# Kernel optimization log

Hardware: AMD Instinct MI355X
Metric: run time of the kernel (lower is better)

## Reference

```python
import jax, jax.numpy as jnp
import numpy as np

MOMENTUM = 0.9


def setup_inputs() -> dict:
    key = jax.random.key(0)
    k1, k2, k3, k4 = jax.random.split(key, 4)
    B, D, C = 524288, 256, 1000
    x = jax.random.normal(k1, (B, D), dtype=jnp.float32)
    l = jax.random.randint(k2, (B,), 0, C, dtype=jnp.int64)
    center_img = jax.random.normal(k3, (C, D), dtype=jnp.float32)
    center_skt = jax.random.normal(k4, (C, D), dtype=jnp.float32)
    return {"x": x, "l": l, "center_img": center_img, "center_skt": center_skt}


def reference(x, l, center_img, center_skt):
    # Faithful vectorized version of CenterAlignment.forward (modality='img').
    # The per-sample Python scatter-add loop -> segment_sum over fixed num_classes;
    # torch.unique's data-dependent class set -> boolean 'present' mask.
    C = center_img.shape[0]
    counts = jax.ops.segment_sum(jnp.ones(x.shape[0], dtype=x.dtype), l, num_segments=C)  # [C]
    sums = jax.ops.segment_sum(x, l, num_segments=C)                                      # [C, D]
    present = counts > 0
    mean = sums / jnp.maximum(counts, 1.0)[:, None]  # per-class mean (safe div for absent classes)
    # momentum update + L2 renormalization, only for classes present in the batch
    upd = center_img * MOMENTUM + mean * (1.0 - MOMENTUM)
    upd = upd / jnp.linalg.norm(upd, axis=1, keepdims=True)
    new_img = jnp.where(present[:, None], upd, center_img)
    # align_loss with alpha=2: mean over present classes of ||c_img - c_skt||^2
    diff = new_img - center_skt
    sq = jnp.sum(diff * diff, axis=1)  # [C]
    n_present = jnp.maximum(jnp.sum(present.astype(x.dtype)), 1.0)
    loss = jnp.sum(jnp.where(present, sq, 0.0)) / n_present
    return loss
```

## Files before the change

kernel.cpp:

```cpp
#include <hip/hip_runtime.h>

#define MAXC    1000
#define DSUB    32
#define LSTR    33
#define THREADS 1024
#define NCHUNK  32
#define FIXS    1048576.0f
#define INVFIXS (1.0f / 1048576.0f)

template <int MODE>
__global__ __launch_bounds__(THREADS) void scatter_kernel(
    const float* __restrict__ x, const int* __restrict__ l,
    float* __restrict__ part, float* __restrict__ cnt_part,
    int* __restrict__ sums_i, int* __restrict__ cnt_i,
    int B, int D, int C, int chunk)
{
    __shared__ int lsum[MAXC * LSTR];
    __shared__ int lcnt[MAXC];

    for (int i = threadIdx.x; i < MAXC * LSTR; i += THREADS) lsum[i] = 0;
    for (int i = threadIdx.x; i < MAXC; i += THREADS) lcnt[i] = 0;
    __syncthreads();

    const bool doCount = (blockIdx.y == 0);
    const int dbase = blockIdx.y * DSUB;
    const int q     = threadIdx.x & 7;
    const int srel  = threadIdx.x >> 3;
    const int STEP  = THREADS >> 3;
    const int DV    = D >> 2;
    const int qb    = (dbase >> 2) + q;

    const float4* __restrict__ x4 = (const float4*)x;

    const int s0 = blockIdx.x * chunk;
    const int s1 = min(B, s0 + chunk);

    int s = s0 + srel;
    for (; s + 3 * STEP < s1; s += 4 * STEP) {
        int c0 = l[s];
        int c1 = l[s + STEP];
        int c2 = l[s + 2 * STEP];
        int c3 = l[s + 3 * STEP];
        float4 v0 = x4[(size_t)s * DV + qb];
        float4 v1 = x4[(size_t)(s + STEP) * DV + qb];
        float4 v2 = x4[(size_t)(s + 2 * STEP) * DV + qb];
        float4 v3 = x4[(size_t)(s + 3 * STEP) * DV + qb];
        const int b0 = c0 * LSTR + (q << 2);
        const int b1 = c1 * LSTR + (q << 2);
        const int b2 = c2 * LSTR + (q << 2);
        const int b3 = c3 * LSTR + (q << 2);
        atomicAdd(&lsum[b0 + 0], __float2int_rn(v0.x * FIXS));
        atomicAdd(&lsum[b0 + 1], __float2int_rn(v0.y * FIXS));
        atomicAdd(&lsum[b0 + 2], __float2int_rn(v0.z * FIXS));
        atomicAdd(&lsum[b0 + 3], __float2int_rn(v0.w * FIXS));
        atomicAdd(&lsum[b1 + 0], __float2int_rn(v1.x * FIXS));
        atomicAdd(&lsum[b1 + 1], __float2int_rn(v1.y * FIXS));
        atomicAdd(&lsum[b1 + 2], __float2int_rn(v1.z * FIXS));
        atomicAdd(&lsum[b1 + 3], __float2int_rn(v1.w * FIXS));
        atomicAdd(&lsum[b2 + 0], __float2int_rn(v2.x * FIXS));
        atomicAdd(&lsum[b2 + 1], __float2int_rn(v2.y * FIXS));
        atomicAdd(&lsum[b2 + 2], __float2int_rn(v2.z * FIXS));
        atomicAdd(&lsum[b2 + 3], __float2int_rn(v2.w * FIXS));
        atomicAdd(&lsum[b3 + 0], __float2int_rn(v3.x * FIXS));
        atomicAdd(&lsum[b3 + 1], __float2int_rn(v3.y * FIXS));
        atomicAdd(&lsum[b3 + 2], __float2int_rn(v3.z * FIXS));
        atomicAdd(&lsum[b3 + 3], __float2int_rn(v3.w * FIXS));
        if (doCount && q == 0) {
            atomicAdd(&lcnt[c0], 1);
            atomicAdd(&lcnt[c1], 1);
            atomicAdd(&lcnt[c2], 1);
            atomicAdd(&lcnt[c3], 1);
        }
    }
    for (; s < s1; s += STEP) {
        int c = l[s];
        float4 v = x4[(size_t)s * DV + qb];
        const int b = c * LSTR + (q << 2);
        atomicAdd(&lsum[b + 0], __float2int_rn(v.x * FIXS));
        atomicAdd(&lsum[b + 1], __float2int_rn(v.y * FIXS));
        atomicAdd(&lsum[b + 2], __float2int_rn(v.z * FIXS));
        atomicAdd(&lsum[b + 3], __float2int_rn(v.w * FIXS));
        if (doCount && q == 0) atomicAdd(&lcnt[c], 1);
    }
    __syncthreads();

    if (MODE == 0) {
        float* myp = part + (size_t)blockIdx.x * C * D + dbase;
        for (int i = threadIdx.x; i < C * DSUB; i += THREADS) {
            const int c = i >> 5, d = i & (DSUB - 1);
            myp[(size_t)c * D + d] = (float)lsum[c * LSTR + d] * INVFIXS;
        }
        if (doCount)
            for (int i = threadIdx.x; i < C; i += THREADS)
                cnt_part[(size_t)blockIdx.x * C + i] = (float)lcnt[i];
    } else {
        for (int i = threadIdx.x; i < C * DSUB; i += THREADS) {
            const int c = i >> 5, d = i & (DSUB - 1);
            const int v = lsum[c * LSTR + d];
            if (v) atomicAdd(&sums_i[(size_t)c * D + dbase + d], v);
        }
        if (doCount)
            for (int i = threadIdx.x; i < C; i += THREADS) {
                const int v = lcnt[i];
                if (v) atomicAdd(&cnt_i[i], v);
            }
    }
}

__device__ __forceinline__ float block_reduce_sum_256(float v, float* sbuf) {
    #pragma unroll
    for (int o = 32; o > 0; o >>= 1) v += __shfl_down(v, o, 64);
    __syncthreads();
    if ((threadIdx.x & 63) == 0) sbuf[threadIdx.x >> 6] = v;
    __syncthreads();
    return sbuf[0] + sbuf[1] + sbuf[2] + sbuf[3];
}

template <int MODE>
__global__ __launch_bounds__(256) void update_kernel(
    const float* __restrict__ part, const float* __restrict__ cnt_part,
    const int* __restrict__ sums_i, const int* __restrict__ cnt_i,
    const float* __restrict__ cimg, const float* __restrict__ cskt,
    float* __restrict__ sq_out, float* __restrict__ pres_out, int C, int D)
{
    __shared__ float sbuf[4];
    __shared__ float cshare;
    const int c = blockIdx.x;
    const int t = threadIdx.x;

    float ssum, cnt;
    if (MODE == 0) {
        ssum = 0.f;
        const float* pc = part + (size_t)c * D + t;
        #pragma unroll
        for (int k = 0; k < NCHUNK; ++k) ssum += pc[(size_t)k * C * D];
        if (t < NCHUNK) {
            float cv = cnt_part[(size_t)t * C + c];
            #pragma unroll
            for (int o = NCHUNK / 2; o > 0; o >>= 1) cv += __shfl_down(cv, o, NCHUNK);
            if (t == 0) cshare = cv;
        }
        __syncthreads();
        cnt = cshare;
    } else {
        ssum = (float)sums_i[(size_t)c * D + t] * INVFIXS;
        if (t == 0) cshare = (float)cnt_i[c];
        __syncthreads();
        cnt = cshare;
    }

    const bool present = cnt > 0.5f;
    const size_t idx = (size_t)c * D + t;
    const float ci = cimg[idx];
    const float cs = cskt[idx];
    const float mean = ssum / fmaxf(cnt, 1.f);
    const float upd = ci * 0.9f + mean * 0.1f;
    const float n2 = block_reduce_sum_256(upd * upd, sbuf);
    const float inv = 1.0f / sqrtf(n2);
    const float newv = present ? upd * inv : ci;
    const float df = newv - cs;
    const float sq = block_reduce_sum_256(df * df, sbuf);
    if (t == 0) {
        sq_out[c]   = present ? sq : 0.f;
        pres_out[c] = present ? 1.f : 0.f;
    }
}

__global__ __launch_bounds__(256) void finalize_kernel(
    const float* __restrict__ sq, const float* __restrict__ pres,
    float* __restrict__ out, int C)
{
    __shared__ float sbuf[4];
    float ls = 0.f, np = 0.f;
    for (int i = threadIdx.x; i < C; i += 256) {
        ls += sq[i];
        np += pres[i];
    }
    ls = block_reduce_sum_256(ls, sbuf);
    np = block_reduce_sum_256(np, sbuf);
    if (threadIdx.x == 0) out[0] = ls / fmaxf(np, 1.f);
}

extern "C" void kernel_launch(void* const* d_in, const int* in_sizes, int n_in,
                              void* d_out, int out_size, void* d_ws, size_t ws_size,
                              hipStream_t stream) {
    const float* x    = (const float*)d_in[0];
    const int*   l    = (const int*)d_in[1];
    const float* cimg = (const float*)d_in[2];
    const float* cskt = (const float*)d_in[3];

    const int B = in_sizes[1];
    const int D = in_sizes[0] / B;
    const int C = in_sizes[2] / D;

    const size_t partElems = (size_t)NCHUNK * C * D;
    const size_t cntElems  = (size_t)NCHUNK * C;
    const size_t need0 = (partElems + cntElems + 2 * (size_t)C) * sizeof(float);

    const int chunk = (B + NCHUNK - 1) / NCHUNK;
    dim3 grid(NCHUNK, D / DSUB);

    if (ws_size >= need0) {
        float* part     = (float*)d_ws;
        float* cnt_part = part + partElems;
        float* sq       = cnt_part + cntElems;
        float* pres     = sq + C;
        scatter_kernel<0><<<grid, THREADS, 0, stream>>>(
            x, l, part, cnt_part, nullptr, nullptr, B, D, C, chunk);
        update_kernel<0><<<C, 256, 0, stream>>>(
            part, cnt_part, nullptr, nullptr, cimg, cskt, sq, pres, C, D);
        finalize_kernel<<<1, 256, 0, stream>>>(sq, pres, (float*)d_out, C);
    } else {
        int*   sums_i = (int*)d_ws;
        int*   cnt_i  = sums_i + (size_t)C * D;
        float* sq     = (float*)(cnt_i + C);
        float* pres   = sq + C;
        hipMemsetAsync(d_ws, 0, sizeof(int) * ((size_t)C * D + C), stream);
        scatter_kernel<1><<<grid, THREADS, 0, stream>>>(
            x, l, nullptr, nullptr, sums_i, cnt_i, B, D, C, chunk);
        update_kernel<1><<<C, 256, 0, stream>>>(
            nullptr, nullptr, sums_i, cnt_i, cimg, cskt, sq, pres, C, D);
        finalize_kernel<<<1, 256, 0, stream>>>(sq, pres, (float*)d_out, C);
    }
}
```

Baseline: 139.5 us.

## Halve scatter D-slice width and software-pipeline loads ahead of LDS atomics

Shrinks each block's feature slice from 32 to 16 columns, which halves the LDS histogram and doubles the grid's y-dimension. It also adds launch bounds asking for more resident blocks per CU. The main loop is software-pipelined so the next four labels and float4 loads are issued before the atomics on the current ones, hiding global memory latency. In exchange, the x rows are read in narrower 64-byte pieces across twice as many blocks, partial-sum writes double, and register pressure rises.

After: 140.6 us. No clear change (+0.8%).

```diff
diff --git a/kernel.cpp b/kernel.cpp
--- a/kernel.cpp
+++ b/kernel.cpp
@@ -1,15 +1,15 @@
 #include <hip/hip_runtime.h>
 
 #define MAXC    1000
-#define DSUB    32
-#define LSTR    33
+#define DSUB    16
+#define LSTR    17
 #define THREADS 1024
 #define NCHUNK  32
 #define FIXS    1048576.0f
 #define INVFIXS (1.0f / 1048576.0f)
 
 template <int MODE>
-__global__ __launch_bounds__(THREADS) void scatter_kernel(
+__global__ __launch_bounds__(THREADS, 8) void scatter_kernel(
     const float* __restrict__ x, const int* __restrict__ l,
     float* __restrict__ part, float* __restrict__ cnt_part,
     int* __restrict__ sums_i, int* __restrict__ cnt_i,
@@ -24,19 +24,28 @@
 
     const bool doCount = (blockIdx.y == 0);
     const int dbase = blockIdx.y * DSUB;
-    const int q     = threadIdx.x & 7;
-    const int srel  = threadIdx.x >> 3;
-    const int STEP  = THREADS >> 3;
-    const int DV    = D >> 2;
-    const int qb    = (dbase >> 2) + q;
+    const int q    = threadIdx.x & 3;
+    const int srel = threadIdx.x >> 2;
+    const int STEP = THREADS >> 2;
+    const int DV   = D >> 2;
+    const int qb   = (dbase >> 2) + q;
 
     const float4* __restrict__ x4 = (const float4*)x;
 
     const int s0 = blockIdx.x * chunk;
     const int s1 = min(B, s0 + chunk);
 
+#define ACC4(cc, vv)                                                   \
+    {                                                                  \
+        const int b_ = (cc) * LSTR + (q << 2);                         \
+        atomicAdd(&lsum[b_ + 0], __float2int_rn((vv).x * FIXS));       \
+        atomicAdd(&lsum[b_ + 1], __float2int_rn((vv).y * FIXS));       \
+        atomicAdd(&lsum[b_ + 2], __float2int_rn((vv).z * FIXS));       \
+        atomicAdd(&lsum[b_ + 3], __float2int_rn((vv).w * FIXS));       \
+    }
+
     int s = s0 + srel;
-    for (; s + 3 * STEP < s1; s += 4 * STEP) {
+    if (s + 3 * STEP < s1) {
         int c0 = l[s];
         int c1 = l[s + STEP];
         int c2 = l[s + 2 * STEP];
@@ -45,41 +54,39 @@
         float4 v1 = x4[(size_t)(s + STEP) * DV + qb];
         float4 v2 = x4[(size_t)(s + 2 * STEP) * DV + qb];
         float4 v3 = x4[(size_t)(s + 3 * STEP) * DV + qb];
-        const int b0 = c0 * LSTR + (q << 2);
-        const int b1 = c1 * LSTR + (q << 2);
-        const int b2 = c2 * LSTR + (q << 2);
-        const int b3 = c3 * LSTR + (q << 2);
-        atomicAdd(&lsum[b0 + 0], __float2int_rn(v0.x * FIXS));
-        atomicAdd(&lsum[b0 + 1], __float2int_rn(v0.y * FIXS));
-        atomicAdd(&lsum[b0 + 2], __float2int_rn(v0.z * FIXS));
-        atomicAdd(&lsum[b0 + 3], __float2int_rn(v0.w * FIXS));
-        atomicAdd(&lsum[b1 + 0], __float2int_rn(v1.x * FIXS));
-        atomicAdd(&lsum[b1 + 1], __float2int_rn(v1.y * FIXS));
-        atomicAdd(&lsum[b1 + 2], __float2int_rn(v1.z * FIXS));
-        atomicAdd(&lsum[b1 + 3], __float2int_rn(v1.w * FIXS));
-        atomicAdd(&lsum[b2 + 0], __float2int_rn(v2.x * FIXS));
-        atomicAdd(&lsum[b2 + 1], __float2int_rn(v2.y * FIXS));
-        atomicAdd(&lsum[b2 + 2], __float2int_rn(v2.z * FIXS));
-        atomicAdd(&lsum[b2 + 3], __float2int_rn(v2.w * FIXS));
-        atomicAdd(&lsum[b3 + 0], __float2int_rn(v3.x * FIXS));
-        atomicAdd(&lsum[b3 + 1], __float2int_rn(v3.y * FIXS));
-        atomicAdd(&lsum[b3 + 2], __float2int_rn(v3.z * FIXS));
-        atomicAdd(&lsum[b3 + 3], __float2int_rn(v3.w * FIXS));
+        int sn = s + 4 * STEP;
+        for (; sn + 3 * STEP < s1; sn += 4 * STEP) {
+            int n0 = l[sn];
+            int n1 = l[sn + STEP];
+            int n2 = l[sn + 2 * STEP];
+            int n3 = l[sn + 3 * STEP];
+            float4 w0 = x4[(size_t)sn * DV + qb];
+            float4 w1 = x4[(size_t)(sn + STEP) * DV + qb];
+            float4 w2 = x4[(size_t)(sn + 2 * STEP) * DV + qb];
+            float4 w3 = x4[(size_t)(sn + 3 * STEP) * DV + qb];
+            ACC4(c0, v0); ACC4(c1, v1); ACC4(c2, v2); ACC4(c3, v3);
+            if (doCount && q == 0) {
+                atomicAdd(&lcnt[c0], 1);
+                atomicAdd(&lcnt[c1], 1);
+                atomicAdd(&lcnt[c2], 1);
+                atomicAdd(&lcnt[c3], 1);
+            }
+            c0 = n0; c1 = n1; c2 = n2; c3 = n3;
+            v0 = w0; v1 = w1; v2 = w2; v3 = w3;
+        }
+        ACC4(c0, v0); ACC4(c1, v1); ACC4(c2, v2); ACC4(c3, v3);
         if (doCount && q == 0) {
             atomicAdd(&lcnt[c0], 1);
             atomicAdd(&lcnt[c1], 1);
             atomicAdd(&lcnt[c2], 1);
             atomicAdd(&lcnt[c3], 1);
         }
+        s = sn;
     }
     for (; s < s1; s += STEP) {
         int c = l[s];
         float4 v = x4[(size_t)s * DV + qb];
-        const int b = c * LSTR + (q << 2);
-        atomicAdd(&lsum[b + 0], __float2int_rn(v.x * FIXS));
-        atomicAdd(&lsum[b + 1], __float2int_rn(v.y * FIXS));
-        atomicAdd(&lsum[b + 2], __float2int_rn(v.z * FIXS));
-        atomicAdd(&lsum[b + 3], __float2int_rn(v.w * FIXS));
+        ACC4(c, v);
         if (doCount && q == 0) atomicAdd(&lcnt[c], 1);
     }
     __syncthreads();
@@ -87,7 +94,7 @@
     if (MODE == 0) {
         float* myp = part + (size_t)blockIdx.x * C * D + dbase;
         for (int i = threadIdx.x; i < C * DSUB; i += THREADS) {
-            const int c = i >> 5, d = i & (DSUB - 1);
+            const int c = i >> 4, d = i & (DSUB - 1);
             myp[(size_t)c * D + d] = (float)lsum[c * LSTR + d] * INVFIXS;
         }
         if (doCount)
@@ -95,7 +102,7 @@
                 cnt_part[(size_t)blockIdx.x * C + i] = (float)lcnt[i];
     } else {
         for (int i = threadIdx.x; i < C * DSUB; i += THREADS) {
-            const int c = i >> 5, d = i & (DSUB - 1);
+            const int c = i >> 4, d = i & (DSUB - 1);
             const int v = lsum[c * LSTR + d];
             if (v) atomicAdd(&sums_i[(size_t)c * D + dbase + d], v);
         }
@@ -105,6 +112,7 @@
                 if (v) atomicAdd(&cnt_i[i], v);
             }
     }
+#undef ACC4
 }
 
 __device__ __forceinline__ float block_reduce_sum_256(float v, float* sbuf) {
```
